# Performance work log

Measured on AMD Instinct MI355X. Metric: run time of the kernel, lower is better.

Reference implementation:

```python
import jax, jax.numpy as jnp
import numpy as np

# RoIAlign config (matches init_kwargs)
OUT_H, OUT_W = 7, 7
SPATIAL_SCALE = 0.25
SAMPLE_NUM = 2  # sampling points per bin side (static)


def setup_inputs() -> dict:
    key = jax.random.key(0)
    k0, k1, k2, k3 = jax.random.split(key, 4)
    B, C, H, W = 2, 256, 200, 336
    N = 1024
    img_h, img_w = H / SPATIAL_SCALE, W / SPATIAL_SCALE
    features = jax.random.normal(k0, (B, C, H, W), dtype=jnp.float32)
    # build valid rois: [batch_idx, x1, y1, x2, y2] in image coordinates
    bidx = jax.random.randint(k1, (N,), 0, B).astype(jnp.float32)
    ctr = jax.random.uniform(k2, (N, 2)) * jnp.array([img_w, img_h], jnp.float32)
    wh = (0.05 + 0.35 * jax.random.uniform(k3, (N, 2))) * jnp.array([img_w, img_h], jnp.float32)
    x1y1 = jnp.clip(ctr - wh / 2, 0.0)
    x2y2 = jnp.minimum(ctr + wh / 2, jnp.array([img_w, img_h], jnp.float32))
    rois = jnp.concatenate([bidx[:, None], x1y1[:, 0:1], x1y1[:, 1:2], x2y2[:, 0:1], x2y2[:, 1:2]], axis=1)
    return {"features": features, "rois": rois}


def _roi_align(features, rois):
    B, C, H, W = features.shape
    N = rois.shape[0]
    ns = SAMPLE_NUM
    P, Q = OUT_H * ns, OUT_W * ns  # full sampling grid per roi

    bidx = rois[:, 0].astype(jnp.int32)
    x1 = rois[:, 1] * SPATIAL_SCALE
    y1 = rois[:, 2] * SPATIAL_SCALE
    x2 = rois[:, 3] * SPATIAL_SCALE
    y2 = rois[:, 4] * SPATIAL_SCALE
    roi_w = jnp.maximum(x2 - x1, 1.0)  # aligned=False legacy semantics
    roi_h = jnp.maximum(y2 - y1, 1.0)
    bin_w = roi_w / OUT_W
    bin_h = roi_h / OUT_H

    # sample coords: y = y1 + (p + 0.5) * bin_h / ns, p in [0, P)
    ys = y1[:, None] + (jnp.arange(P, dtype=jnp.float32) + 0.5) * (bin_h[:, None] / ns)  # (N,P)
    xs = x1[:, None] + (jnp.arange(Q, dtype=jnp.float32) + 0.5) * (bin_w[:, None] / ns)  # (N,Q)

    # out-of-bound samples contribute zero (kernel skips y<-1 or y>H)
    ymask = (ys >= -1.0) & (ys <= H)
    xmask = (xs >= -1.0) & (xs <= W)
    y = jnp.clip(ys, 0.0, H - 1)
    x = jnp.clip(xs, 0.0, W - 1)
    y0 = jnp.floor(y).astype(jnp.int32)
    x0 = jnp.floor(x).astype(jnp.int32)
    y1i = jnp.minimum(y0 + 1, H - 1)
    x1i = jnp.minimum(x0 + 1, W - 1)
    ly = y - y0.astype(jnp.float32)
    lx = x - x0.astype(jnp.float32)
    hy, hx = 1.0 - ly, 1.0 - lx

    b = bidx[:, None, None]            # (N,1,1)
    def gather(yi, xi):                # -> (N,P,Q,C)
        return features[b, :, yi[:, :, None], xi[:, None, :]]
    f00 = gather(y0, x0)
    f01 = gather(y0, x1i)
    f10 = gather(y1i, x0)
    f11 = gather(y1i, x1i)

    wy0, wy1 = hy[:, :, None, None], ly[:, :, None, None]  # (N,P,1,1)
    wx0, wx1 = hx[:, None, :, None], lx[:, None, :, None]  # (N,1,Q,1)
    val = wy0 * (wx0 * f00 + wx1 * f01) + wy1 * (wx0 * f10 + wx1 * f11)
    val = val * (ymask[:, :, None, None] & xmask[:, None, :, None])

    # average the ns x ns samples per output bin
    val = val.reshape(N, OUT_H, ns, OUT_W, ns, C).mean(axis=(2, 4))  # (N,OUT_H,OUT_W,C)
    return jnp.transpose(val, (0, 3, 1, 2))  # (N,C,OUT_H,OUT_W)


def reference(features, rois):
    return _roi_align(features, rois)
```

## Files before the change

### kernel.cpp

```cpp
#include <hip/hip_runtime.h>
#include <hip/hip_fp16.h>

#define BB   2
#define CCH  256
#define HH   200
#define WW   336
#define HWN  (HH * WW)
#define OH   7
#define OW   7
#define SCALEF 0.25f
#define NBIN (OH * OW)
#define PER_ROI (CCH * NBIN)
#define NBANDS 8
#define NBUCK (BB * NBANDS)

typedef float  nfloat4 __attribute__((ext_vector_type(4)));

__device__ __forceinline__ __half2 u32_as_h2(unsigned int u) {
    union { unsigned int u; __half2 h; } c;
    c.u = u;
    return c.h;
}

__global__ __launch_bounds__(1024) void roi_sort_k(const float* __restrict__ rois,
                                                   int N, int* __restrict__ perm) {
    const int tid = threadIdx.x;
    if (N > 1024 || N < 8) {
        for (int i = tid; i < N; i += blockDim.x) perm[i] = i;
        return;
    }
    __shared__ int cnt[NBUCK], off[NBUCK];
    __shared__ unsigned char keys[1024];
    if (tid < NBUCK) cnt[tid] = 0;
    __syncthreads();
    for (int i = tid; i < N; i += blockDim.x) {
        const float* r = rois + i * 5;
        const int b = (int)r[0];
        const float yc = (r[2] + r[4]) * 0.5f * SCALEF;
        int band = (int)(yc * ((float)NBANDS / (float)HH));
        band = min(max(band, 0), NBANDS - 1);
        const int k = b * NBANDS + band;
        keys[i] = (unsigned char)k;
        atomicAdd(&cnt[k], 1);
    }
    __syncthreads();
    if (tid == 0) {
        int s = 0;
        for (int k = 0; k < NBUCK; ++k) { off[k] = s; s += cnt[k]; }
    }
    __syncthreads();
    for (int i = tid; i < N; i += blockDim.x) {
        const int pos = atomicAdd(&off[keys[i]], 1);
        perm[pos] = i;
    }
}

__global__ __launch_bounds__(256) void transpose_f16_k(const float* __restrict__ src,
                                                       unsigned short* __restrict__ dst) {
    __shared__ float tile[64][65];
    const int b   = blockIdx.z;
    const int hw0 = blockIdx.x * 64;
    const int c0  = blockIdx.y * 64;
    const int tx  = threadIdx.x;
    const int ty  = threadIdx.y;

#pragma unroll
    for (int r = 0; r < 4; ++r) {
        const int cl = ty + r * 16;
        const nfloat4 v = __builtin_nontemporal_load(
            (const nfloat4*)(src + (size_t)(b * CCH + c0 + cl) * HWN + hw0 + tx * 4));
        tile[cl][tx * 4 + 0] = v.x;
        tile[cl][tx * 4 + 1] = v.y;
        tile[cl][tx * 4 + 2] = v.z;
        tile[cl][tx * 4 + 3] = v.w;
    }
    __syncthreads();
#pragma unroll
    for (int r = 0; r < 4; ++r) {
        const int hwl = ty + r * 16;
        ushort4 o;
        o.x = __half_as_ushort(__float2half(tile[tx * 4 + 0][hwl]));
        o.y = __half_as_ushort(__float2half(tile[tx * 4 + 1][hwl]));
        o.z = __half_as_ushort(__float2half(tile[tx * 4 + 2][hwl]));
        o.w = __half_as_ushort(__float2half(tile[tx * 4 + 3][hwl]));
        *(ushort4*)(dst + (size_t)(b * HWN + hw0 + hwl) * CCH + c0 + tx * 4) = o;
    }
}

__global__ __launch_bounds__(512, 8) void roi_align_f16_k(const unsigned short* __restrict__ f,
                                                          const float* __restrict__ rois,
                                                          const int* __restrict__ perm,
                                                          float* __restrict__ out) {
    const int nblk = gridDim.x;
    int p;
    if ((nblk & 7) == 0) {
        p = (blockIdx.x & 7) * (nblk >> 3) + (blockIdx.x >> 3);
    } else {
        p = blockIdx.x;
    }
    const int n    = perm[p];
    const int tid  = threadIdx.x;
    const int lane = tid & 63;
    const int g    = tid >> 6;
    const int c4   = lane * 4;

    __shared__ __align__(16) unsigned short buf_h[PER_ROI];
    __shared__ int   s_yb0[14], s_yb1[14];
    __shared__ int   s_xb0[14], s_xb1[14];
    __shared__ float s_ly[14],  s_lx[14];
    __shared__ float s_vy[14],  s_vx[14];

    const float* r = rois + n * 5;
    const int   b   = (int)r[0];
    const float rx1 = r[1] * SCALEF, ry1 = r[2] * SCALEF;
    const float rx2 = r[3] * SCALEF, ry2 = r[4] * SCALEF;
    const float bw = fmaxf(rx2 - rx1, 1.0f) * (1.0f / OW);
    const float bh = fmaxf(ry2 - ry1, 1.0f) * (1.0f / OH);

    if (tid < 14) {
        const float ys = ry1 + ((float)tid + 0.5f) * (bh * 0.5f);
        s_vy[tid] = (ys >= -1.0f && ys <= (float)HH) ? 1.0f : 0.0f;
        const float y = fminf(fmaxf(ys, 0.0f), (float)(HH - 1));
        const int y0  = (int)floorf(y);
        const int y1  = min(y0 + 1, HH - 1);
        s_yb0[tid] = (b * HH + y0) * (WW * CCH);
        s_yb1[tid] = (b * HH + y1) * (WW * CCH);
        s_ly[tid]  = y - (float)y0;
    } else if (tid >= 64 && tid < 78) {
        const int j = tid - 64;
        const float xs = rx1 + ((float)j + 0.5f) * (bw * 0.5f);
        s_vx[j] = (xs >= -1.0f && xs <= (float)WW) ? 1.0f : 0.0f;
        const float x = fminf(fmaxf(xs, 0.0f), (float)(WW - 1));
        const int x0  = (int)floorf(x);
        const int x1  = min(x0 + 1, WW - 1);
        s_xb0[j] = x0 * CCH;
        s_xb1[j] = x1 * CCH;
        s_lx[j]  = x - (float)x0;
    }
    __syncthreads();

    const unsigned short* fb = f + c4;

    for (int bin = g; bin < NBIN; bin += 8) {
        const int ph = bin / OW;
        const int pw = bin - ph * OW;
        float accx = 0.0f, accy = 0.0f, accz = 0.0f, accw = 0.0f;
#pragma unroll
        for (int ix = 0; ix < 2; ++ix) {
            const int px  = pw * 2 + ix;
            const int xb0 = s_xb0[px], xb1 = s_xb1[px];
            const float lx = s_lx[px];
            const float mv = s_vx[px] * 0.25f;
            const __half2 HX = __float2half2_rn(1.0f - lx);
            const __half2 LX = __float2half2_rn(lx);
#pragma unroll
            for (int iy = 0; iy < 2; ++iy) {
                const int py  = ph * 2 + iy;
                const int yb0 = s_yb0[py], yb1 = s_yb1[py];
                const float ly = s_ly[py];
                const float m  = mv * s_vy[py];
                const uint2 q00 = *(const uint2*)(fb + yb0 + xb0);
                const uint2 q01 = *(const uint2*)(fb + yb0 + xb1);
                const uint2 q10 = *(const uint2*)(fb + yb1 + xb0);
                const uint2 q11 = *(const uint2*)(fb + yb1 + xb1);
                const __half2 r0a = __hfma2(LX, u32_as_h2(q01.x), __hmul2(HX, u32_as_h2(q00.x)));
                const __half2 r0b = __hfma2(LX, u32_as_h2(q01.y), __hmul2(HX, u32_as_h2(q00.y)));
                const __half2 r1a = __hfma2(LX, u32_as_h2(q11.x), __hmul2(HX, u32_as_h2(q10.x)));
                const __half2 r1b = __hfma2(LX, u32_as_h2(q11.y), __hmul2(HX, u32_as_h2(q10.y)));
                const __half2 MH0 = __float2half2_rn(m * (1.0f - ly));
                const __half2 MH1 = __float2half2_rn(m * ly);
                const __half2 vA = __hfma2(MH1, r1a, __hmul2(MH0, r0a));
                const __half2 vB = __hfma2(MH1, r1b, __hmul2(MH0, r0b));
                accx += __low2float(vA);
                accy += __high2float(vA);
                accz += __low2float(vB);
                accw += __high2float(vB);
            }
        }
        buf_h[(c4 + 0) * NBIN + bin] = __half_as_ushort(__float2half(accx));
        buf_h[(c4 + 1) * NBIN + bin] = __half_as_ushort(__float2half(accy));
        buf_h[(c4 + 2) * NBIN + bin] = __half_as_ushort(__float2half(accz));
        buf_h[(c4 + 3) * NBIN + bin] = __half_as_ushort(__float2half(accw));
    }
    __syncthreads();

    nfloat4* ob = (nfloat4*)(out + (size_t)n * PER_ROI);
    const uint2* bb = (const uint2*)buf_h;
    for (int i = tid; i < PER_ROI / 4; i += 512) {
        const uint2 q = bb[i];
        const __half2 a = u32_as_h2(q.x), c = u32_as_h2(q.y);
        nfloat4 v;
        v.x = __low2float(a);  v.y = __high2float(a);
        v.z = __low2float(c);  v.w = __high2float(c);
        __builtin_nontemporal_store(v, ob + i);
    }
}

__global__ __launch_bounds__(256) void roi_align_direct_k(const float* __restrict__ f,
                                                          const float* __restrict__ rois,
                                                          float* __restrict__ out) {
    const int n   = blockIdx.x;
    const int c   = threadIdx.x;

    __shared__ int   s_y0[14], s_y1[14], s_x0[14], s_x1[14];
    __shared__ float s_ly[14], s_lx[14], s_vy[14], s_vx[14];

    const float* r = rois + n * 5;
    const int   b   = (int)r[0];
    const float rx1 = r[1] * SCALEF, ry1 = r[2] * SCALEF;
    const float rx2 = r[3] * SCALEF, ry2 = r[4] * SCALEF;
    const float bw = fmaxf(rx2 - rx1, 1.0f) * (1.0f / OW);
    const float bh = fmaxf(ry2 - ry1, 1.0f) * (1.0f / OH);

    if (c < 14) {
        const float ys = ry1 + ((float)c + 0.5f) * (bh * 0.5f);
        s_vy[c] = (ys >= -1.0f && ys <= (float)HH) ? 1.0f : 0.0f;
        const float y = fminf(fmaxf(ys, 0.0f), (float)(HH - 1));
        const int y0  = (int)floorf(y);
        s_y0[c] = y0 * WW;
        s_y1[c] = min(y0 + 1, HH - 1) * WW;
        s_ly[c] = y - (float)y0;
    } else if (c >= 64 && c < 78) {
        const int j = c - 64;
        const float xs = rx1 + ((float)j + 0.5f) * (bw * 0.5f);
        s_vx[j] = (xs >= -1.0f && xs <= (float)WW) ? 1.0f : 0.0f;
        const float x = fminf(fmaxf(xs, 0.0f), (float)(WW - 1));
        const int x0  = (int)floorf(x);
        s_x0[j] = x0;
        s_x1[j] = min(x0 + 1, WW - 1);
        s_lx[j] = x - (float)x0;
    }
    __syncthreads();

    const float* fb = f + (size_t)(b * CCH + c) * HWN;
    for (int bin = 0; bin < NBIN; ++bin) {
        const int ph = bin / OW, pw = bin - ph * OW;
        float acc = 0.0f;
        for (int iy = 0; iy < 2; ++iy) {
            const int py = ph * 2 + iy;
            const float ly = s_ly[py], hy = 1.0f - ly;
            for (int ix = 0; ix < 2; ++ix) {
                const int px = pw * 2 + ix;
                const float lx = s_lx[px], hx = 1.0f - lx;
                const float m = s_vy[py] * s_vx[px] * 0.25f;
                acc += m * (hy * (hx * fb[s_y0[py] + s_x0[px]] + lx * fb[s_y0[py] + s_x1[px]]) +
                            ly * (hx * fb[s_y1[py] + s_x0[px]] + lx * fb[s_y1[py] + s_x1[px]]));
            }
        }
        out[(size_t)n * PER_ROI + c * NBIN + bin] = acc;
    }
}

extern "C" void kernel_launch(void* const* d_in, const int* in_sizes, int n_in,
                              void* d_out, int out_size, void* d_ws, size_t ws_size,
                              hipStream_t stream) {
    const float* feat = (const float*)d_in[0];
    const float* rois = (const float*)d_in[1];
    float* out = (float*)d_out;
    const int N = in_sizes[1] / 5;

    const size_t tensor_bytes = (size_t)BB * CCH * HWN * sizeof(unsigned short);
    const size_t need = tensor_bytes + (size_t)N * sizeof(int);
    if (ws_size >= need) {
        unsigned short* fcl = (unsigned short*)d_ws;
        int* perm = (int*)((char*)d_ws + tensor_bytes);
        roi_sort_k<<<1, 1024, 0, stream>>>(rois, N, perm);
        transpose_f16_k<<<dim3(HWN / 64, CCH / 64, BB), dim3(16, 16), 0, stream>>>(feat, fcl);
        roi_align_f16_k<<<N, 512, 0, stream>>>(fcl, rois, perm, out);
    } else {
        roi_align_direct_k<<<N, 256, 0, stream>>>(feat, rois, out);
    }
}
```

Measured before the change: 244.4 us.

## Fold ROI sort into transpose kernel and split lanes across x-corners with 16B loads

Result: faster. 239.5 us (-2.0%).

```diff
diff --git a/kernel.cpp b/kernel.cpp
--- a/kernel.cpp
+++ b/kernel.cpp
@@ -22,47 +22,50 @@
     return c.h;
 }
 
-__global__ __launch_bounds__(1024) void roi_sort_k(const float* __restrict__ rois,
-                                                   int N, int* __restrict__ perm) {
-    const int tid = threadIdx.x;
-    if (N > 1024 || N < 8) {
-        for (int i = tid; i < N; i += blockDim.x) perm[i] = i;
-        return;
-    }
+__global__ __launch_bounds__(256) void transpose_f16_k(const float* __restrict__ src,
+                                                       unsigned short* __restrict__ dst,
+                                                       const float* __restrict__ rois,
+                                                       int N, int* __restrict__ perm) {
+    __shared__ float tile[64][65];
     __shared__ int cnt[NBUCK], off[NBUCK];
     __shared__ unsigned char keys[1024];
-    if (tid < NBUCK) cnt[tid] = 0;
-    __syncthreads();
-    for (int i = tid; i < N; i += blockDim.x) {
-        const float* r = rois + i * 5;
-        const int b = (int)r[0];
-        const float yc = (r[2] + r[4]) * 0.5f * SCALEF;
-        int band = (int)(yc * ((float)NBANDS / (float)HH));
-        band = min(max(band, 0), NBANDS - 1);
-        const int k = b * NBANDS + band;
-        keys[i] = (unsigned char)k;
-        atomicAdd(&cnt[k], 1);
-    }
-    __syncthreads();
-    if (tid == 0) {
-        int s = 0;
-        for (int k = 0; k < NBUCK; ++k) { off[k] = s; s += cnt[k]; }
-    }
-    __syncthreads();
-    for (int i = tid; i < N; i += blockDim.x) {
-        const int pos = atomicAdd(&off[keys[i]], 1);
-        perm[pos] = i;
-    }
-}
-
-__global__ __launch_bounds__(256) void transpose_f16_k(const float* __restrict__ src,
-                                                       unsigned short* __restrict__ dst) {
-    __shared__ float tile[64][65];
+
+    const int tx  = threadIdx.x;
+    const int ty  = threadIdx.y;
+    const int tid = ty * 16 + tx;
+
+    if (blockIdx.x == 0 && blockIdx.y == 0 && blockIdx.z == 0) {
+        if (N > 1024 || N < 8) {
+            for (int i = tid; i < N; i += 256) perm[i] = i;
+        } else {
+            if (tid < NBUCK) cnt[tid] = 0;
+            __syncthreads();
+            for (int i = tid; i < N; i += 256) {
+                const float* r = rois + i * 5;
+                const int b = (int)r[0];
+                const float yc = (r[2] + r[4]) * 0.5f * SCALEF;
+                int band = (int)(yc * ((float)NBANDS / (float)HH));
+                band = min(max(band, 0), NBANDS - 1);
+                const int k = b * NBANDS + band;
+                keys[i] = (unsigned char)k;
+                atomicAdd(&cnt[k], 1);
+            }
+            __syncthreads();
+            if (tid == 0) {
+                int s = 0;
+                for (int k = 0; k < NBUCK; ++k) { off[k] = s; s += cnt[k]; }
+            }
+            __syncthreads();
+            for (int i = tid; i < N; i += 256) {
+                perm[atomicAdd(&off[keys[i]], 1)] = i;
+            }
+        }
+        __syncthreads();
+    }
+
     const int b   = blockIdx.z;
     const int hw0 = blockIdx.x * 64;
     const int c0  = blockIdx.y * 64;
-    const int tx  = threadIdx.x;
-    const int ty  = threadIdx.y;
 
 #pragma unroll
     for (int r = 0; r < 4; ++r) {
@@ -101,8 +104,10 @@
     const int n    = perm[p];
     const int tid  = threadIdx.x;
     const int lane = tid & 63;
+    const int half = lane >> 5;
+    const int l32  = lane & 31;
     const int g    = tid >> 6;
-    const int c4   = lane * 4;
+    const int c8   = l32 * 8;
 
     __shared__ __align__(16) unsigned short buf_h[PER_ROI];
     __shared__ int   s_yb0[14], s_yb1[14];
@@ -139,48 +144,45 @@
     }
     __syncthreads();
 
-    const unsigned short* fb = f + c4;
+    const unsigned short* fp = f + c8;
 
     for (int bin = g; bin < NBIN; bin += 8) {
         const int ph = bin / OW;
         const int pw = bin - ph * OW;
-        float accx = 0.0f, accy = 0.0f, accz = 0.0f, accw = 0.0f;
+        float acc[8] = {0.f, 0.f, 0.f, 0.f, 0.f, 0.f, 0.f, 0.f};
 #pragma unroll
         for (int ix = 0; ix < 2; ++ix) {
             const int px  = pw * 2 + ix;
-            const int xb0 = s_xb0[px], xb1 = s_xb1[px];
-            const float lx = s_lx[px];
-            const float mv = s_vx[px] * 0.25f;
-            const __half2 HX = __float2half2_rn(1.0f - lx);
-            const __half2 LX = __float2half2_rn(lx);
+            const int xbs = half ? s_xb1[px] : s_xb0[px];
+            const float wxs = (half ? s_lx[px] : (1.0f - s_lx[px]))
+                              * s_vx[px] * 0.25f;
 #pragma unroll
             for (int iy = 0; iy < 2; ++iy) {
-                const int py  = ph * 2 + iy;
-                const int yb0 = s_yb0[py], yb1 = s_yb1[py];
+                const int py = ph * 2 + iy;
                 const float ly = s_ly[py];
-                const float m  = mv * s_vy[py];
-                const uint2 q00 = *(const uint2*)(fb + yb0 + xb0);
-                const uint2 q01 = *(const uint2*)(fb + yb0 + xb1);
-                const uint2 q10 = *(const uint2*)(fb + yb1 + xb0);
-                const uint2 q11 = *(const uint2*)(fb + yb1 + xb1);
-                const __half2 r0a = __hfma2(LX, u32_as_h2(q01.x), __hmul2(HX, u32_as_h2(q00.x)));
-                const __half2 r0b = __hfma2(LX, u32_as_h2(q01.y), __hmul2(HX, u32_as_h2(q00.y)));
-                const __half2 r1a = __hfma2(LX, u32_as_h2(q11.x), __hmul2(HX, u32_as_h2(q10.x)));
-                const __half2 r1b = __hfma2(LX, u32_as_h2(q11.y), __hmul2(HX, u32_as_h2(q10.y)));
-                const __half2 MH0 = __float2half2_rn(m * (1.0f - ly));
-                const __half2 MH1 = __float2half2_rn(m * ly);
-                const __half2 vA = __hfma2(MH1, r1a, __hmul2(MH0, r0a));
-                const __half2 vB = __hfma2(MH1, r1b, __hmul2(MH0, r0b));
-                accx += __low2float(vA);
-                accy += __high2float(vA);
-                accz += __low2float(vB);
-                accw += __high2float(vB);
-            }
-        }
-        buf_h[(c4 + 0) * NBIN + bin] = __half_as_ushort(__float2half(accx));
-        buf_h[(c4 + 1) * NBIN + bin] = __half_as_ushort(__float2half(accy));
-        buf_h[(c4 + 2) * NBIN + bin] = __half_as_ushort(__float2half(accz));
-        buf_h[(c4 + 3) * NBIN + bin] = __half_as_ushort(__float2half(accw));
+                const float m  = wxs * s_vy[py];
+                const uint4 q0 = *(const uint4*)(fp + s_yb0[py] + xbs);
+                const uint4 q1 = *(const uint4*)(fp + s_yb1[py] + xbs);
+                const __half2 W0 = __float2half2_rn(m * (1.0f - ly));
+                const __half2 W1 = __float2half2_rn(m * ly);
+                const __half2 v0 = __hfma2(W1, u32_as_h2(q1.x), __hmul2(W0, u32_as_h2(q0.x)));
+                const __half2 v1 = __hfma2(W1, u32_as_h2(q1.y), __hmul2(W0, u32_as_h2(q0.y)));
+                const __half2 v2 = __hfma2(W1, u32_as_h2(q1.z), __hmul2(W0, u32_as_h2(q0.z)));
+                const __half2 v3 = __hfma2(W1, u32_as_h2(q1.w), __hmul2(W0, u32_as_h2(q0.w)));
+                acc[0] += __low2float(v0);  acc[1] += __high2float(v0);
+                acc[2] += __low2float(v1);  acc[3] += __high2float(v1);
+                acc[4] += __low2float(v2);  acc[5] += __high2float(v2);
+                acc[6] += __low2float(v3);  acc[7] += __high2float(v3);
+            }
+        }
+#pragma unroll
+        for (int j = 0; j < 8; ++j) {
+            acc[j] += __shfl_xor(acc[j], 32);
+        }
+#pragma unroll
+        for (int j = 0; j < 8; ++j) {
+            buf_h[(c8 + j) * NBIN + bin] = __half_as_ushort(__float2half(acc[j]));
+        }
     }
     __syncthreads();
 
@@ -264,8 +266,8 @@
     if (ws_size >= need) {
         unsigned short* fcl = (unsigned short*)d_ws;
         int* perm = (int*)((char*)d_ws + tensor_bytes);
-        roi_sort_k<<<1, 1024, 0, stream>>>(rois, N, perm);
-        transpose_f16_k<<<dim3(HWN / 64, CCH / 64, BB), dim3(16, 16), 0, stream>>>(feat, fcl);
+        transpose_f16_k<<<dim3(HWN / 64, CCH / 64, BB), dim3(16, 16), 0, stream>>>(
+            feat, fcl, rois, N, perm);
         roi_align_f16_k<<<N, 512, 0, stream>>>(fcl, rois, perm, out);
     } else {
         roi_align_direct_k<<<N, 256, 0, stream>>>(feat, rois, out);
```
